# Kernel tuning notes

Measured on AMD Instinct MI355X. Metric: run time of the kernel, lower is better.

## Reference

```python
import jax, jax.numpy as jnp
import numpy as np


def _dequant4(qweight, scales, qzeros, groupsize):
    """GPTQ int4 dequant.
    qweight: (K//8, N) int32, 8 int4 values packed along K (low nibble = lowest k).
    scales:  (G, N) float, G = K // groupsize.
    qzeros:  (G, N//8) int32, 8 int4 zeros packed along N.
    Returns dense (K, N) float weight: w*scale - (z+1)*scale, per the kernel.
    """
    K8, N = qweight.shape
    shifts = jnp.arange(8, dtype=jnp.int32) * 4
    # unpack weights along K: (K//8, 8, N) -> (K, N)
    w = (qweight[:, None, :] >> shifts[None, :, None]) & 15
    w = w.reshape(K8 * 8, N).astype(scales.dtype)
    # unpack zeros along N: (G, N//8, 8) -> (G, N)
    z = (qzeros[:, :, None] >> shifts[None, None, :]) & 15
    z = z.reshape(qzeros.shape[0], N).astype(scales.dtype)
    zero_term = (z + 1.0) * scales  # (G, N)
    # broadcast each group's scale/zero over its groupsize rows of K
    sc_k = jnp.repeat(scales, groupsize, axis=0)      # (K, N)
    zt_k = jnp.repeat(zero_term, groupsize, axis=0)   # (K, N)
    return w * sc_k - zt_k


def setup_inputs() -> dict:
    key = jax.random.key(0)
    ks = jax.random.split(key, 10)
    B, S, K, N = 2, 2048, 4096, 11008
    gs = 128
    G_gu = K // gs        # 32
    G_d = N // gs         # 86
    hi = jnp.int32(1073741823)
    x = jax.random.normal(ks[0], (B, S, K), dtype=jnp.float32)
    gate_qweight = jax.random.randint(ks[1], (K // 8, N), 0, hi, dtype=jnp.int32)
    gate_scales = jax.random.uniform(ks[2], (G_gu, N), dtype=jnp.float32) * 0.01
    gate_qzeros = jax.random.randint(ks[3], (G_gu, N // 8), 0, hi, dtype=jnp.int32)
    up_qweight = jax.random.randint(ks[4], (K // 8, N), 0, hi, dtype=jnp.int32)
    up_scales = jax.random.uniform(ks[5], (G_gu, N), dtype=jnp.float32) * 0.01
    up_qzeros = jax.random.randint(ks[6], (G_gu, N // 8), 0, hi, dtype=jnp.int32)
    down_qweight = jax.random.randint(ks[7], (N // 8, K), 0, hi, dtype=jnp.int32)
    down_scales = jax.random.uniform(ks[8], (G_d, K), dtype=jnp.float32) * 0.01
    down_qzeros = jax.random.randint(ks[9], (G_d, K // 8), 0, hi, dtype=jnp.int32)
    return {
        "x": x,
        "gate_qweight": gate_qweight, "gate_scales": gate_scales, "gate_qzeros": gate_qzeros,
        "up_qweight": up_qweight, "up_scales": up_scales, "up_qzeros": up_qzeros,
        "down_qweight": down_qweight, "down_scales": down_scales, "down_qzeros": down_qzeros,
        "groupsize": gs,
    }


def reference(x, gate_qweight, gate_scales, gate_qzeros,
              up_qweight, up_scales, up_qzeros,
              down_qweight, down_scales, down_qzeros, groupsize):
    Wg = _dequant4(gate_qweight, gate_scales, gate_qzeros, groupsize)  # (K, N)
    Wu = _dequant4(up_qweight, up_scales, up_qzeros, groupsize)        # (K, N)
    g = jnp.einsum('bsk,kn->bsn', x, Wg)
    u = jnp.einsum('bsk,kn->bsn', x, Wu)
    h = jax.nn.silu(g) * u                                             # (B, S, N)
    Wd = _dequant4(down_qweight, down_scales, down_qzeros, groupsize)  # (N, K)
    return jnp.einsum('bsn,nk->bsk', h, Wd)
```

## Files before the change

kernel.cpp:

```cpp
#include <hip/hip_runtime.h>
#include <hip/hip_bf16.h>

static constexpr int M  = 4096;
static constexpr int K  = 4096;
static constexpr int NN = 11008;

typedef _Float16 f16;
typedef _Float16 f16x2 __attribute__((ext_vector_type(2)));
typedef _Float16 f16x8 __attribute__((ext_vector_type(8)));
typedef float    f32x4 __attribute__((ext_vector_type(4)));

union dq_u { f16x2 h[4]; f16x8 v; };

__device__ __forceinline__ f16x8 dq8(unsigned q, f16x2 s2, f16x2 zc2) {
    dq_u u;
    unsigned t0 = ( q         & 0x000F000Fu) | 0x64006400u;
    unsigned t1 = ((q >> 4)   & 0x000F000Fu) | 0x64006400u;
    unsigned t2 = ((q >> 8)   & 0x000F000Fu) | 0x64006400u;
    unsigned t3 = ((q >> 12)  & 0x000F000Fu) | 0x64006400u;
    u.h[0] = (__builtin_bit_cast(f16x2, t0) - zc2) * s2;
    u.h[1] = (__builtin_bit_cast(f16x2, t1) - zc2) * s2;
    u.h[2] = (__builtin_bit_cast(f16x2, t2) - zc2) * s2;
    u.h[3] = (__builtin_bit_cast(f16x2, t3) - zc2) * s2;
    return u.v;
}

__device__ __forceinline__ void gll16(const f16* g, f16* l) {
    __builtin_amdgcn_global_load_lds(
        (const __attribute__((address_space(1))) unsigned int*)g,
        (__attribute__((address_space(3))) unsigned int*)l,
        16, 0, 0);
}

__global__ __launch_bounds__(256) void convert_x_kernel(
    const float* __restrict__ x, f16* __restrict__ xp)
{
    size_t i = ((size_t)blockIdx.x * 256 + threadIdx.x) * 8;
    float4 f0 = *(const float4*)(x + i);
    float4 f1 = *(const float4*)(x + i + 4);
    f16x8 v;
    v[0] = (f16)f0.x; v[1] = (f16)f1.x;
    v[2] = (f16)f0.y; v[3] = (f16)f1.y;
    v[4] = (f16)f0.z; v[5] = (f16)f1.z;
    v[6] = (f16)f0.w; v[7] = (f16)f1.w;
    *(f16x8*)(xp + i) = v;
}

__global__ __launch_bounds__(256) void dequant_gu_strip(
    const int* __restrict__ gqw, const float* __restrict__ gsc, const int* __restrict__ gqz,
    const int* __restrict__ uqw, const float* __restrict__ usc, const int* __restrict__ uqz,
    f16* __restrict__ wc, int n0)
{
    int nl = blockIdx.x * 256 + threadIdx.x;
    int n  = n0 + nl;
    int k0 = blockIdx.y * 32;
    int g  = k0 >> 7;
    int sh = (n & 7) * 4;

    float sgf = gsc[(size_t)g * NN + n];
    float suf = usc[(size_t)g * NN + n];
    int zg = (gqz[(size_t)g * (NN / 8) + (n >> 3)] >> sh) & 15;
    int zu = (uqz[(size_t)g * (NN / 8) + (n >> 3)] >> sh) & 15;
    f16 sgh = (f16)sgf, suh = (f16)suf;
    f16 zcg = (f16)(float)(1025 + zg);
    f16 zcu = (f16)(float)(1025 + zu);
    f16x2 s2g = {sgh, sgh}, zc2g = {zcg, zcg};
    f16x2 s2u = {suh, suh}, zc2u = {zcu, zcu};

    size_t jg = (size_t)((nl >> 4) * 32 + (nl & 15));
    size_t ju = jg + 16;

#pragma unroll
    for (int i = 0; i < 4; ++i) {
        unsigned qg = (unsigned)gqw[(size_t)(k0 / 8 + i) * NN + n];
        unsigned qu = (unsigned)uqw[(size_t)(k0 / 8 + i) * NN + n];
        *(f16x8*)&wc[jg * K + k0 + i * 8] = dq8(qg, s2g, zc2g);
        *(f16x8*)&wc[ju * K + k0 + i * 8] = dq8(qu, s2u, zc2u);
    }
}

__global__ __launch_bounds__(256) void dequant_d_strip(
    const int* __restrict__ dqw, const float* __restrict__ dsc, const int* __restrict__ dqz,
    f16* __restrict__ wd, int c0)
{
    int cl = blockIdx.x * 256 + threadIdx.x;
    int c  = c0 + cl;
    int n0 = blockIdx.y * 32;
    int g  = n0 >> 7;
    int sh = (c & 7) * 4;

    float sf = dsc[(size_t)g * K + c];
    int   z  = (dqz[(size_t)g * (K / 8) + (c >> 3)] >> sh) & 15;
    f16 shh = (f16)sf;
    f16 zch = (f16)(float)(1025 + z);
    f16x2 s2 = {shh, shh}, zc2 = {zch, zch};

#pragma unroll
    for (int i = 0; i < 4; ++i) {
        unsigned q = (unsigned)dqw[(size_t)(n0 / 8 + i) * K + c];
        *(f16x8*)&wd[(size_t)cl * NN + n0 + i * 8] = dq8(q, s2, zc2);
    }
}

template<int EPI>
__global__ __launch_bounds__(512) void gemm8p(
    const f16* __restrict__ Ag,
    const f16* __restrict__ Bg,
    void*      __restrict__ Cv,
    const int SK, const int NT, const int cbase)
{
    __shared__ __align__(16) f16 LA[2][2][128 * 64];
    __shared__ __align__(16) f16 LB[2][2][128 * 64];

    const int tid  = threadIdx.x;
    const int lane = tid & 63;
    const int wave = tid >> 6;
    const int wm   = wave >> 2;
    const int wbh  = (wave >> 1) & 1;
    const int wnq  = wave & 1;
    const int quad = lane >> 4;
    const int lr   = lane & 15;

    const int GX  = gridDim.x, GY = gridDim.y;
    const int nwg = GX * GY;
    const int lin = blockIdx.y * GX + blockIdx.x;
    const int q8  = nwg >> 3, r8 = nwg & 7;
    const int xcd = lin & 7, ldx = lin >> 3;
    const int s   = (xcd < r8 ? xcd * (q8 + 1)
                              : r8 * (q8 + 1) + (xcd - r8) * q8) + ldx;
    const int span = 4 * GY;
    const int mb   = (s / span) * 4 + (s & 3);
    const int cb   = (s % span) >> 2;

    const int m0  = mb * 256;
    const int nb0 = cb * 256;

    const int trow = tid >> 3;
    const int tch  = (tid & 7) ^ (trow & 7);
    const size_t arow = (size_t)(m0  + trow) * SK + (size_t)tch * 8;
    const size_t brow = (size_t)(nb0 + trow) * SK + (size_t)tch * 8;
    const int lstg = wave * 512;

    const int c0e = ((quad) ^ (lr & 7)) * 8;
    const int c1e = ((4 + quad) ^ (lr & 7)) * 8;

    f32x4 acc[8][4];
#pragma unroll
    for (int i = 0; i < 8; ++i)
#pragma unroll
        for (int j = 0; j < 4; ++j) acc[i][j] = (f32x4){0.f, 0.f, 0.f, 0.f};

    f16x8 a_[2][4];
    f16x8 b_[2][2][2];

#define STAGE_A(D_, H_, T_) do {                                              \
    const f16* s_ = Ag + arow + (size_t)(H_) * 128 * SK + (size_t)(T_) * 64;  \
    gll16(s_, &LA[D_][H_][lstg]);                                             \
    gll16(s_ + (size_t)64 * SK, &LA[D_][H_][4096 + lstg]); } while (0)

#define STAGE_B(D_, H_, T_) do {                                              \
    const f16* s_ = Bg + brow + (size_t)(H_) * 128 * SK + (size_t)(T_) * 64;  \
    gll16(s_, &LB[D_][H_][lstg]);                                             \
    gll16(s_ + (size_t)64 * SK, &LB[D_][H_][4096 + lstg]); } while (0)

#define LOAD_A(D_, MH_) do {                                                  \
    _Pragma("unroll")                                                         \
    for (int mt = 0; mt < 4; ++mt) {                                          \
        a_[0][mt] = *(const f16x8*)&LA[D_][wm][((MH_) * 64 + mt * 16 + lr) * 64 + c0e]; \
        a_[1][mt] = *(const f16x8*)&LA[D_][wm][((MH_) * 64 + mt * 16 + lr) * 64 + c1e]; \
    } } while (0)

#define LOAD_B(D_, NH_) do {                                                  \
    _Pragma("unroll")                                                         \
    for (int n2 = 0; n2 < 2; ++n2) {                                          \
        b_[NH_][0][n2] = *(const f16x8*)&LB[D_][wbh][(wnq * 64 + (NH_) * 32 + n2 * 16 + lr) * 64 + c0e]; \
        b_[NH_][1][n2] = *(const f16x8*)&LB[D_][wbh][(wnq * 64 + (NH_) * 32 + n2 * 16 + lr) * 64 + c1e]; \
    } } while (0)

#define QMFMA(MH_, NH_) do {                                                  \
    __builtin_amdgcn_s_setprio(1);                                            \
    _Pragma("unroll")                                                         \
    for (int kk = 0; kk < 2; ++kk)                                            \
    _Pragma("unroll")                                                         \
    for (int n2 = 0; n2 < 2; ++n2)                                            \
    _Pragma("unroll")                                                         \
    for (int mt = 0; mt < 4; ++mt)                                            \
        acc[(MH_) * 4 + mt][(NH_) * 2 + n2] =                                 \
            __builtin_amdgcn_mfma_f32_16x16x32_f16(                           \
                a_[kk][mt], b_[NH_][kk][n2],                                  \
                acc[(MH_) * 4 + mt][(NH_) * 2 + n2], 0, 0, 0);                \
    __builtin_amdgcn_s_setprio(0); } while (0)

#define BAR() do { __builtin_amdgcn_s_barrier();                              \
                   __builtin_amdgcn_sched_barrier(0); } while (0)
#define WAITV6() do { asm volatile("s_waitcnt vmcnt(6)" ::: "memory");        \
                      __builtin_amdgcn_sched_barrier(0); } while (0)
#define WAITV0() do { asm volatile("s_waitcnt vmcnt(0)" ::: "memory");        \
                      __builtin_amdgcn_sched_barrier(0); } while (0)

    STAGE_A(0, 0, 0); STAGE_A(0, 1, 0); STAGE_B(0, 0, 0); STAGE_B(0, 1, 0);
    if (NT > 1) { STAGE_B(1, 0, 1); STAGE_A(1, 0, 1); STAGE_A(1, 1, 1); }
    if (NT > 1) { WAITV6(); } else { WAITV0(); }
    BAR();

#pragma unroll 2
    for (int t = 0; t < NT; ++t) {
        const int d  = t & 1;
        const int dn = d ^ 1;
        const bool s1 = (t + 1 < NT);
        const bool s2 = (t + 2 < NT);

        LOAD_A(d, 0);
        LOAD_B(d, 0);
        if (s1) STAGE_B(dn, 1, t + 1);
        QMFMA(0, 0);
        BAR();
        LOAD_B(d, 1);
        QMFMA(0, 1);
        BAR();
        LOAD_A(d, 1);
        if (s2) STAGE_B(d, 0, t + 2);
        QMFMA(1, 0);
        BAR();
        if (s2) { STAGE_A(d, 0, t + 2); STAGE_A(d, 1, t + 2); }
        QMFMA(1, 1);
        if (s2) { WAITV6(); } else { WAITV0(); }
        BAR();
    }

    if constexpr (EPI == 0) {
        f16* __restrict__ h = (f16*)Cv;
        const int jw = cbase + nb0 + wbh * 128 + wnq * 64;
#pragma unroll
        for (int p = 0; p < 2; ++p) {
            const int nbase = ((jw + p * 32) >> 5) * 16;
            const int n  = nbase + lr;
            const int np = (n & ~7) | (((n & 3) << 1) | ((n >> 2) & 1));
#pragma unroll
            for (int mt8 = 0; mt8 < 8; ++mt8)
#pragma unroll
                for (int r = 0; r < 4; ++r) {
                    const int m = m0 + wm * 128 + mt8 * 16 + quad * 4 + r;
                    float gv = acc[mt8][2 * p][r];
                    float uv = acc[mt8][2 * p + 1][r];
                    float hv = (gv / (1.0f + __expf(-gv))) * uv;
                    h[(size_t)m * NN + np] = (f16)hv;
                }
        }
    } else {
        float* __restrict__ out = (float*)Cv;
        const int cw = cbase + nb0 + wbh * 128 + wnq * 64;
#pragma unroll
        for (int nt = 0; nt < 4; ++nt)
#pragma unroll
            for (int mt8 = 0; mt8 < 8; ++mt8)
#pragma unroll
                for (int r = 0; r < 4; ++r) {
                    const int m = m0 + wm * 128 + mt8 * 16 + quad * 4 + r;
                    out[(size_t)m * K + cw + nt * 16 + lr] = acc[mt8][nt][r];
                }
    }

#undef STAGE_A
#undef STAGE_B
#undef LOAD_A
#undef LOAD_B
#undef QMFMA
#undef BAR
#undef WAITV6
#undef WAITV0
}

extern "C" void kernel_launch(void* const* d_in, const int* in_sizes, int n_in,
                              void* d_out, int out_size, void* d_ws, size_t ws_size,
                              hipStream_t stream) {
    const float* x   = (const float*)d_in[0];
    const int*   gqw = (const int*)d_in[1];
    const float* gsc = (const float*)d_in[2];
    const int*   gqz = (const int*)d_in[3];
    const int*   uqw = (const int*)d_in[4];
    const float* usc = (const float*)d_in[5];
    const int*   uqz = (const int*)d_in[6];
    const int*   dqw = (const int*)d_in[7];
    const float* dsc = (const float*)d_in[8];
    const int*   dqz = (const int*)d_in[9];
    float* out = (float*)d_out;

    const size_t HB = (size_t)M * NN * 2;
    char* ws = (char*)d_ws;
    f16* h  = (f16*)ws;
    f16* xp = (f16*)(ws + HB);

    convert_x_kernel<<<(M * K / 8) / 256, 256, 0, stream>>>(x, xp);

    const int JC = 8192;
    for (int j0 = 0; j0 < 2 * NN; j0 += JC) {
        int jc  = 2 * NN - j0 < JC ? 2 * NN - j0 : JC;
        int n0  = j0 >> 1;
        int ncn = jc >> 1;
        f16* wc = (f16*)d_out;
        dequant_gu_strip<<<dim3(ncn / 256, K / 32), 256, 0, stream>>>(
            gqw, gsc, gqz, uqw, usc, uqz, wc, n0);
        gemm8p<0><<<dim3(M / 256, jc / 256), 512, 0, stream>>>(
            xp, wc, (void*)h, K, K / 64, j0);
    }

    size_t availD = ws_size - HB;
    int KC = (int)(availD / ((size_t)NN * 2));
    KC &= ~255;
    if (KC > K) KC = K;
    if (KC < 256) KC = 256;
    f16* wd = (f16*)(ws + HB);
    for (int c0 = 0; c0 < K; c0 += KC) {
        int kc = K - c0 < KC ? K - c0 : KC;
        dequant_d_strip<<<dim3(kc / 256, NN / 32), 256, 0, stream>>>(
            dqw, dsc, dqz, wd, c0);
        gemm8p<1><<<dim3(M / 256, kc / 256), 512, 0, stream>>>(
            h, wd, out, NN, NN / 64, c0);
    }
}
```

Baseline: 1.329 ms.

## Restructure GEMM pipeline with explicit LDS waitcnts and extra barriers

Changes the software pipeline in the 8-phase GEMM: both B halves for the next-next tile are now staged in the same phase instead of splitting B(1) into the next iteration, and the global wait is raised from vmcnt(6) to vmcnt(8) to match. Explicit lgkmcnt waits and extra workgroup barriers are placed between LDS fragment loads and MFMA clusters, so the compiler cannot interleave them unpredictably. The aim is a more regular overlap of LDS reads, global staging and matrix math. The cost is twice as many barriers per iteration, which can stall waves, and a changed stage ordering that must stay correct with respect to buffer reuse. The down-projection grid expression is rewritten to an equivalent value.

```diff
diff --git a/kernel.cpp b/kernel.cpp
--- a/kernel.cpp
+++ b/kernel.cpp
@@ -191,40 +191,51 @@
                 acc[(MH_) * 4 + mt][(NH_) * 2 + n2], 0, 0, 0);                \
     __builtin_amdgcn_s_setprio(0); } while (0)
 
-#define BAR() do { __builtin_amdgcn_s_barrier();                              \
+#define BAR() do { __builtin_amdgcn_sched_barrier(0);                         \
+                   __builtin_amdgcn_s_barrier();                              \
                    __builtin_amdgcn_sched_barrier(0); } while (0)
-#define WAITV6() do { asm volatile("s_waitcnt vmcnt(6)" ::: "memory");        \
+#define LGKM8() do { asm volatile("s_waitcnt lgkmcnt(8)" ::: "memory");       \
+                     __builtin_amdgcn_sched_barrier(0); } while (0)
+#define LGKM0() do { asm volatile("s_waitcnt lgkmcnt(0)" ::: "memory");       \
+                     __builtin_amdgcn_sched_barrier(0); } while (0)
+#define WAITV8() do { asm volatile("s_waitcnt vmcnt(8)" ::: "memory");        \
                       __builtin_amdgcn_sched_barrier(0); } while (0)
 #define WAITV0() do { asm volatile("s_waitcnt vmcnt(0)" ::: "memory");        \
                       __builtin_amdgcn_sched_barrier(0); } while (0)
 
     STAGE_A(0, 0, 0); STAGE_A(0, 1, 0); STAGE_B(0, 0, 0); STAGE_B(0, 1, 0);
-    if (NT > 1) { STAGE_B(1, 0, 1); STAGE_A(1, 0, 1); STAGE_A(1, 1, 1); }
-    if (NT > 1) { WAITV6(); } else { WAITV0(); }
+    if (NT > 1) { STAGE_B(1, 0, 1); STAGE_B(1, 1, 1);
+                  STAGE_A(1, 0, 1); STAGE_A(1, 1, 1); }
+    if (NT > 1) { WAITV8(); } else { WAITV0(); }
     BAR();
 
 #pragma unroll 2
     for (int t = 0; t < NT; ++t) {
         const int d  = t & 1;
-        const int dn = d ^ 1;
-        const bool s1 = (t + 1 < NT);
         const bool s2 = (t + 2 < NT);
 
         LOAD_A(d, 0);
         LOAD_B(d, 0);
-        if (s1) STAGE_B(dn, 1, t + 1);
+        LGKM8();
+        BAR();
+        LGKM0();
         QMFMA(0, 0);
         BAR();
         LOAD_B(d, 1);
+        BAR();
+        LGKM0();
         QMFMA(0, 1);
         BAR();
         LOAD_A(d, 1);
-        if (s2) STAGE_B(d, 0, t + 2);
+        if (s2) { STAGE_B(d, 0, t + 2); STAGE_B(d, 1, t + 2); }
+        BAR();
+        LGKM0();
         QMFMA(1, 0);
         BAR();
         if (s2) { STAGE_A(d, 0, t + 2); STAGE_A(d, 1, t + 2); }
+        BAR();
         QMFMA(1, 1);
-        if (s2) { WAITV6(); } else { WAITV0(); }
+        if (s2) { WAITV8(); } else { WAITV0(); }
         BAR();
     }
 
@@ -267,7 +278,9 @@
 #undef LOAD_B
 #undef QMFMA
 #undef BAR
-#undef WAITV6
+#undef LGKM8
+#undef LGKM0
+#undef WAITV8
 #undef WAITV0
 }
 
@@ -315,7 +328,7 @@
         int kc = K - c0 < KC ? K - c0 : KC;
         dequant_d_strip<<<dim3(kc / 256, NN / 32), 256, 0, stream>>>(
             dqw, dsc, dqz, wd, c0);
-        gemm8p<1><<<dim3(M / 256, kc / 256), 512, 0, stream>>>(
+        gemm8p<1><<<dim3(M / 256, kc / 128 / 2), 512, 0, stream>>>(
             h, wd, out, NN, NN / 64, c0);
     }
 }
```

After: 1.385 ms. 1.04x slower.

## Switch GEMM inner loop from 16x16x32 to 32x32x16 MFMA tiles

Applied to the files above, without the earlier changes.

Replaces the 16x16x32 f16 MFMA micro-tiles with 32x32x16 MFMAs. LDS fragment loads, accumulator layout, epilogue row mapping and the gate/up interleave in the dequant kernel all change to match. The aim is fewer LDS reads per FLOP and fewer MFMA issues per k-step, since larger tiles reuse each loaded fragment more. In exchange, register usage and the LDS access pattern change, and the swizzle may now produce bank conflicts.

```diff
diff --git a/kernel.cpp b/kernel.cpp
--- a/kernel.cpp
+++ b/kernel.cpp
@@ -9,6 +9,7 @@
 typedef _Float16 f16x2 __attribute__((ext_vector_type(2)));
 typedef _Float16 f16x8 __attribute__((ext_vector_type(8)));
 typedef float    f32x4 __attribute__((ext_vector_type(4)));
+typedef float    f32x16 __attribute__((ext_vector_type(16)));
 
 union dq_u { f16x2 h[4]; f16x8 v; };
 
@@ -67,8 +68,8 @@
     f16x2 s2g = {sgh, sgh}, zc2g = {zcg, zcg};
     f16x2 s2u = {suh, suh}, zc2u = {zcu, zcu};
 
-    size_t jg = (size_t)((nl >> 4) * 32 + (nl & 15));
-    size_t ju = jg + 16;
+    size_t jg = (size_t)((nl >> 5) * 64 + (nl & 31));
+    size_t ju = jg + 32;
 
 #pragma unroll
     for (int i = 0; i < 4; ++i) {
@@ -118,8 +119,8 @@
     const int wm   = wave >> 2;
     const int wbh  = (wave >> 1) & 1;
     const int wnq  = wave & 1;
-    const int quad = lane >> 4;
-    const int lr   = lane & 15;
+    const int lr32 = lane & 31;
+    const int hi   = lane >> 5;
 
     const int GX  = gridDim.x, GY = gridDim.y;
     const int nwg = GX * GY;
@@ -141,17 +142,21 @@
     const size_t brow = (size_t)(nb0 + trow) * SK + (size_t)tch * 8;
     const int lstg = wave * 512;
 
-    const int c0e = ((quad) ^ (lr & 7)) * 8;
-    const int c1e = ((4 + quad) ^ (lr & 7)) * 8;
-
-    f32x4 acc[8][4];
-#pragma unroll
-    for (int i = 0; i < 8; ++i)
-#pragma unroll
-        for (int j = 0; j < 4; ++j) acc[i][j] = (f32x4){0.f, 0.f, 0.f, 0.f};
+    int ce[4];
+#pragma unroll
+    for (int ks = 0; ks < 4; ++ks)
+        ce[ks] = ((ks * 2 + hi) ^ (lr32 & 7)) * 8;
+
+    f32x16 acc[4][2];
+#pragma unroll
+    for (int i = 0; i < 4; ++i)
+#pragma unroll
+        for (int j = 0; j < 2; ++j)
+#pragma unroll
+            for (int r = 0; r < 16; ++r) acc[i][j][r] = 0.f;
 
     f16x8 a_[2][4];
-    f16x8 b_[2][2][2];
+    f16x8 b_[2][4];
 
 #define STAGE_A(D_, H_, T_) do {                                              \
     const f16* s_ = Ag + arow + (size_t)(H_) * 128 * SK + (size_t)(T_) * 64;  \
@@ -165,30 +170,31 @@
 
 #define LOAD_A(D_, MH_) do {                                                  \
     _Pragma("unroll")                                                         \
-    for (int mt = 0; mt < 4; ++mt) {                                          \
-        a_[0][mt] = *(const f16x8*)&LA[D_][wm][((MH_) * 64 + mt * 16 + lr) * 64 + c0e]; \
-        a_[1][mt] = *(const f16x8*)&LA[D_][wm][((MH_) * 64 + mt * 16 + lr) * 64 + c1e]; \
+    for (int mt = 0; mt < 2; ++mt) {                                          \
+        const f16* base_ = &LA[D_][wm][((MH_) * 64 + mt * 32 + lr32) * 64];   \
+        _Pragma("unroll")                                                     \
+        for (int ks = 0; ks < 4; ++ks)                                        \
+            a_[mt][ks] = *(const f16x8*)&base_[ce[ks]];                       \
     } } while (0)
 
-#define LOAD_B(D_, NH_) do {                                                  \
-    _Pragma("unroll")                                                         \
-    for (int n2 = 0; n2 < 2; ++n2) {                                          \
-        b_[NH_][0][n2] = *(const f16x8*)&LB[D_][wbh][(wnq * 64 + (NH_) * 32 + n2 * 16 + lr) * 64 + c0e]; \
-        b_[NH_][1][n2] = *(const f16x8*)&LB[D_][wbh][(wnq * 64 + (NH_) * 32 + n2 * 16 + lr) * 64 + c1e]; \
+#define LOAD_B(D_, NT_) do {                                                  \
+    {                                                                         \
+        const f16* base_ = &LB[D_][wbh][(wnq * 64 + (NT_) * 32 + lr32) * 64]; \
+        _Pragma("unroll")                                                     \
+        for (int ks = 0; ks < 4; ++ks)                                        \
+            b_[NT_][ks] = *(const f16x8*)&base_[ce[ks]];                      \
     } } while (0)
 
-#define QMFMA(MH_, NH_) do {                                                  \
+#define QMFMA(MH_, NT_) do {                                                  \
     __builtin_amdgcn_s_setprio(1);                                            \
     _Pragma("unroll")                                                         \
-    for (int kk = 0; kk < 2; ++kk)                                            \
+    for (int ks = 0; ks < 4; ++ks)                                            \
     _Pragma("unroll")                                                         \
-    for (int n2 = 0; n2 < 2; ++n2)                                            \
-    _Pragma("unroll")                                                         \
-    for (int mt = 0; mt < 4; ++mt)                                            \
-        acc[(MH_) * 4 + mt][(NH_) * 2 + n2] =                                 \
-            __builtin_amdgcn_mfma_f32_16x16x32_f16(                           \
-                a_[kk][mt], b_[NH_][kk][n2],                                  \
-                acc[(MH_) * 4 + mt][(NH_) * 2 + n2], 0, 0, 0);                \
+    for (int mt = 0; mt < 2; ++mt)                                            \
+        acc[(MH_) * 2 + mt][NT_] =                                            \
+            __builtin_amdgcn_mfma_f32_32x32x16_f16(                           \
+                a_[mt][ks], b_[NT_][ks],                                      \
+                acc[(MH_) * 2 + mt][NT_], 0, 0, 0);                           \
     __builtin_amdgcn_s_setprio(0); } while (0)
 
 #define BAR() do { __builtin_amdgcn_s_barrier();                              \
@@ -231,33 +237,31 @@
     if constexpr (EPI == 0) {
         f16* __restrict__ h = (f16*)Cv;
         const int jw = cbase + nb0 + wbh * 128 + wnq * 64;
-#pragma unroll
-        for (int p = 0; p < 2; ++p) {
-            const int nbase = ((jw + p * 32) >> 5) * 16;
-            const int n  = nbase + lr;
-            const int np = (n & ~7) | (((n & 3) << 1) | ((n >> 2) & 1));
-#pragma unroll
-            for (int mt8 = 0; mt8 < 8; ++mt8)
-#pragma unroll
-                for (int r = 0; r < 4; ++r) {
-                    const int m = m0 + wm * 128 + mt8 * 16 + quad * 4 + r;
-                    float gv = acc[mt8][2 * p][r];
-                    float uv = acc[mt8][2 * p + 1][r];
-                    float hv = (gv / (1.0f + __expf(-gv))) * uv;
-                    h[(size_t)m * NN + np] = (f16)hv;
-                }
-        }
+        const int n  = (jw >> 6) * 32 + lr32;
+        const int np = (n & ~7) | (((n & 3) << 1) | ((n >> 2) & 1));
+#pragma unroll
+        for (int fi = 0; fi < 4; ++fi)
+#pragma unroll
+            for (int r = 0; r < 16; ++r) {
+                const int m = m0 + wm * 128 + fi * 32
+                            + (r & 3) + 8 * (r >> 2) + 4 * hi;
+                float gv = acc[fi][0][r];
+                float uv = acc[fi][1][r];
+                float hv = (gv / (1.0f + __expf(-gv))) * uv;
+                h[(size_t)m * NN + np] = (f16)hv;
+            }
     } else {
         float* __restrict__ out = (float*)Cv;
         const int cw = cbase + nb0 + wbh * 128 + wnq * 64;
 #pragma unroll
-        for (int nt = 0; nt < 4; ++nt)
-#pragma unroll
-            for (int mt8 = 0; mt8 < 8; ++mt8)
-#pragma unroll
-                for (int r = 0; r < 4; ++r) {
-                    const int m = m0 + wm * 128 + mt8 * 16 + quad * 4 + r;
-                    out[(size_t)m * K + cw + nt * 16 + lr] = acc[mt8][nt][r];
+        for (int fi = 0; fi < 4; ++fi)
+#pragma unroll
+            for (int nt = 0; nt < 2; ++nt)
+#pragma unroll
+                for (int r = 0; r < 16; ++r) {
+                    const int m = m0 + wm * 128 + fi * 32
+                                + (r & 3) + 8 * (r >> 2) + 4 * hi;
+                    out[(size_t)m * K + cw + nt * 32 + lr32] = acc[fi][nt][r];
                 }
     }
 
```

New measurement: 1.454 ms. 1.09x slower.

## Simplify GEMM mainloop to load-all-then-compute with full-tile double buffering

Applied to the files above, without the earlier changes.

Restructures the GEMM main loop. The old schedule interleaved LDS fragment loads, partial global stages and MFMA quarters across four barriers per iteration. Now each iteration reads all A and B fragments from LDS first, runs all 64 MFMAs at raised priority, then issues the whole next-next tile's global-to-LDS stages, with two barriers per iteration. This cuts barrier count and scheduling complexity, but needs double the A fragment registers and gives less overlap between LDS reads and MFMA, which may raise register pressure or expose latency.

```diff
diff --git a/kernel.cpp b/kernel.cpp
--- a/kernel.cpp
+++ b/kernel.cpp
@@ -150,7 +150,7 @@
 #pragma unroll
         for (int j = 0; j < 4; ++j) acc[i][j] = (f32x4){0.f, 0.f, 0.f, 0.f};
 
-    f16x8 a_[2][4];
+    f16x8 a_[2][2][4];
     f16x8 b_[2][2][2];
 
 #define STAGE_A(D_, H_, T_) do {                                              \
@@ -166,8 +166,8 @@
 #define LOAD_A(D_, MH_) do {                                                  \
     _Pragma("unroll")                                                         \
     for (int mt = 0; mt < 4; ++mt) {                                          \
-        a_[0][mt] = *(const f16x8*)&LA[D_][wm][((MH_) * 64 + mt * 16 + lr) * 64 + c0e]; \
-        a_[1][mt] = *(const f16x8*)&LA[D_][wm][((MH_) * 64 + mt * 16 + lr) * 64 + c1e]; \
+        a_[MH_][0][mt] = *(const f16x8*)&LA[D_][wm][((MH_) * 64 + mt * 16 + lr) * 64 + c0e]; \
+        a_[MH_][1][mt] = *(const f16x8*)&LA[D_][wm][((MH_) * 64 + mt * 16 + lr) * 64 + c1e]; \
     } } while (0)
 
 #define LOAD_B(D_, NH_) do {                                                  \
@@ -178,7 +178,6 @@
     } } while (0)
 
 #define QMFMA(MH_, NH_) do {                                                  \
-    __builtin_amdgcn_s_setprio(1);                                            \
     _Pragma("unroll")                                                         \
     for (int kk = 0; kk < 2; ++kk)                                            \
     _Pragma("unroll")                                                         \
@@ -187,44 +186,44 @@
     for (int mt = 0; mt < 4; ++mt)                                            \
         acc[(MH_) * 4 + mt][(NH_) * 2 + n2] =                                 \
             __builtin_amdgcn_mfma_f32_16x16x32_f16(                           \
-                a_[kk][mt], b_[NH_][kk][n2],                                  \
+                a_[MH_][kk][mt], b_[NH_][kk][n2],                             \
                 acc[(MH_) * 4 + mt][(NH_) * 2 + n2], 0, 0, 0);                \
-    __builtin_amdgcn_s_setprio(0); } while (0)
-
-#define BAR() do { __builtin_amdgcn_s_barrier();                              \
+    } while (0)
+
+#define BAR() do { __builtin_amdgcn_sched_barrier(0);                         \
+                   __builtin_amdgcn_s_barrier();                              \
                    __builtin_amdgcn_sched_barrier(0); } while (0)
-#define WAITV6() do { asm volatile("s_waitcnt vmcnt(6)" ::: "memory");        \
+#define WAITV8() do { asm volatile("s_waitcnt vmcnt(8)" ::: "memory");        \
                       __builtin_amdgcn_sched_barrier(0); } while (0)
 #define WAITV0() do { asm volatile("s_waitcnt vmcnt(0)" ::: "memory");        \
                       __builtin_amdgcn_sched_barrier(0); } while (0)
 
     STAGE_A(0, 0, 0); STAGE_A(0, 1, 0); STAGE_B(0, 0, 0); STAGE_B(0, 1, 0);
-    if (NT > 1) { STAGE_B(1, 0, 1); STAGE_A(1, 0, 1); STAGE_A(1, 1, 1); }
-    if (NT > 1) { WAITV6(); } else { WAITV0(); }
+    if (NT > 1) { STAGE_A(1, 0, 1); STAGE_A(1, 1, 1);
+                  STAGE_B(1, 0, 1); STAGE_B(1, 1, 1); }
+    if (NT > 1) { WAITV8(); } else { WAITV0(); }
     BAR();
 
 #pragma unroll 2
     for (int t = 0; t < NT; ++t) {
         const int d  = t & 1;
-        const int dn = d ^ 1;
         const bool s1 = (t + 1 < NT);
         const bool s2 = (t + 2 < NT);
 
         LOAD_A(d, 0);
         LOAD_B(d, 0);
-        if (s1) STAGE_B(dn, 1, t + 1);
+        LOAD_A(d, 1);
+        LOAD_B(d, 1);
+        __builtin_amdgcn_s_setprio(1);
         QMFMA(0, 0);
+        QMFMA(0, 1);
+        QMFMA(1, 0);
+        QMFMA(1, 1);
+        __builtin_amdgcn_s_setprio(0);
         BAR();
-        LOAD_B(d, 1);
-        QMFMA(0, 1);
-        BAR();
-        LOAD_A(d, 1);
-        if (s2) STAGE_B(d, 0, t + 2);
-        QMFMA(1, 0);
-        BAR();
-        if (s2) { STAGE_A(d, 0, t + 2); STAGE_A(d, 1, t + 2); }
-        QMFMA(1, 1);
-        if (s2) { WAITV6(); } else { WAITV0(); }
+        if (s2) { STAGE_A(d, 0, t + 2); STAGE_A(d, 1, t + 2);
+                  STAGE_B(d, 0, t + 2); STAGE_B(d, 1, t + 2); }
+        if (s1) { if (s2) { WAITV8(); } else { WAITV0(); } }
         BAR();
     }
 
@@ -267,7 +266,7 @@
 #undef LOAD_B
 #undef QMFMA
 #undef BAR
-#undef WAITV6
+#undef WAITV8
 #undef WAITV0
 }
 
```

Measured after the change: 1.405 ms. 1.06x slower.
